# Performance work log

Measured on AMD Instinct MI355X. Metric: run time of the kernel, lower is better.

Reference implementation:

```python
import jax, jax.numpy as jnp
import numpy as np

N = 8192
K = 15


def setup_inputs() -> dict:
    key = jax.random.key(0)
    kx, ky = jax.random.split(key)
    x = jax.random.normal(kx, (N, 2), dtype=jnp.float32)
    y = jax.random.randint(ky, (N,), 0, 2, dtype=jnp.int32)
    return {"x": x, "y": y}


def reference(x, y):
    # Pairwise squared Euclidean distances via ||a||^2 + ||b||^2 - 2 a.b
    n = x.shape[0]
    xx = jnp.sum(x * x, axis=-1)                      # [n]
    d = xx[:, None] + xx[None, :] - 2.0 * (x @ x.T)   # [n, n]
    # exclude self (the original loop skips i == j)
    idx = jnp.arange(n)
    d = d.at[idx, idx].set(jnp.inf)
    # K nearest neighbors per point (smallest distances)
    _, knn_idx = jax.lax.top_k(-d, K)                 # [n, K]
    knn_labels = y[knn_idx].astype(jnp.float32)       # [n, K]
    # majority vote: sum of K binary labels > K/2 -> class 1
    out = (jnp.sum(knn_labels, axis=-1) > (K / 2)).astype(jnp.float32)
    return out
```

## Files before the change

### kernel.cpp

```cpp
#include <hip/hip_runtime.h>

#define NPTS 8192
#define KNN  15
#define QPW  4
#define WPB  8
#define TPB  (WPB * 64)

__device__ __forceinline__ int prefix_below(unsigned long long m) {
  return (int)__builtin_amdgcn_mbcnt_hi((unsigned int)(m >> 32),
            __builtin_amdgcn_mbcnt_lo((unsigned int)m, 0u));
}

__device__ __forceinline__ unsigned int bitonic_sort_u32(unsigned int v, int lane) {
#pragma unroll
  for (int k = 2; k <= 64; k <<= 1) {
#pragma unroll
    for (int j = k >> 1; j > 0; j >>= 1) {
      unsigned int o = __shfl_xor(v, j, 64);
      bool keep_min = ((lane & k) == 0) == ((lane & j) == 0);
      unsigned int lo = (v < o) ? v : o;
      unsigned int hi = (v < o) ? o : v;
      v = keep_min ? lo : hi;
    }
  }
  return v;
}

__device__ __forceinline__ unsigned long long bitonic_sort_u64(unsigned long long v, int lane) {
#pragma unroll
  for (int k = 2; k <= 64; k <<= 1) {
#pragma unroll
    for (int j = k >> 1; j > 0; j >>= 1) {
      unsigned long long o = __shfl_xor(v, j, 64);
      bool keep_min = ((lane & k) == 0) == ((lane & j) == 0);
      unsigned long long lo = (v < o) ? v : o;
      unsigned long long hi = (v < o) ? o : v;
      v = keep_min ? lo : hi;
    }
  }
  return v;
}

__global__ __launch_bounds__(TPB)
void knn_kernel(const float* __restrict__ x, const int* __restrict__ y,
                float* __restrict__ out) {
  __shared__ float4 sx4[NPTS / 2];
  __shared__ unsigned int ybits[NPTS / 32];
  __shared__ unsigned int buf[WPB][QPW][64];

  const int tid = threadIdx.x;

  const float4* gx4 = (const float4*)x;
#pragma unroll
  for (int i = tid; i < NPTS / 2; i += TPB) sx4[i] = gx4[i];
  if (tid < NPTS / 32) {
    const int4* yy = (const int4*)(y + (tid << 5));
    unsigned int b = 0;
#pragma unroll
    for (int k2 = 0; k2 < 8; ++k2) {
      int4 v = yy[k2];
      b |= ((unsigned int)(v.x & 1) << (4 * k2)) |
           ((unsigned int)(v.y & 1) << (4 * k2 + 1)) |
           ((unsigned int)(v.z & 1) << (4 * k2 + 2)) |
           ((unsigned int)(v.w & 1) << (4 * k2 + 3));
    }
    ybits[tid] = b;
  }
  __syncthreads();

  const int w = tid >> 6;
  const int lane = tid & 63;
  const int q0 = ((int)blockIdx.x * WPB + w) * QPW;

  float qx[QPW], qy[QPW];
#pragma unroll
  for (int qi = 0; qi < QPW; ++qi) {
    float2 xq = ((const float2*)sx4)[q0 + qi];
    qx[qi] = xq.x; qy[qi] = xq.y;
  }

  float m0[QPW], m1[QPW];
#pragma unroll
  for (int qi = 0; qi < QPW; ++qi) { m0[qi] = 3.0e38f; m1[qi] = 3.0e38f; }

#pragma unroll 8
  for (int s = 0; s < 64; ++s) {
    float4 p = sx4[(s << 6) + lane];
#pragma unroll
    for (int qi = 0; qi < QPW; ++qi) {
      float dx0 = qx[qi] - p.x, dy0 = qy[qi] - p.y;
      float dx1 = qx[qi] - p.z, dy1 = qy[qi] - p.w;
      float d0 = __builtin_fmaf(dx0, dx0, dy0 * dy0);
      float d1 = __builtin_fmaf(dx1, dx1, dy1 * dy1);
      m0[qi] = fminf(m0[qi], d0);
      m1[qi] = fminf(m1[qi], d1);
    }
  }

  float T[QPW];
#pragma unroll
  for (int qi = 0; qi < QPW; ++qi) {
    unsigned int s = bitonic_sort_u32(__float_as_uint(fminf(m0[qi], m1[qi])), lane);
    T[qi] = __uint_as_float(__shfl(s, KNN, 64)) * (1.0f + 1.0e-5f) + 1.0e-30f;
  }

  int cnt[QPW];
#pragma unroll
  for (int qi = 0; qi < QPW; ++qi) cnt[qi] = 0;

#pragma unroll 4
  for (int s = 0; s < 64; ++s) {
    float4 p = sx4[(s << 6) + lane];
    int j0 = ((s << 6) + lane) << 1;
#pragma unroll
    for (int qi = 0; qi < QPW; ++qi) {
      float dx0 = qx[qi] - p.x, dy0 = qy[qi] - p.y;
      float dx1 = qx[qi] - p.z, dy1 = qy[qi] - p.w;
      float d0 = __builtin_fmaf(dx0, dx0, dy0 * dy0);
      float d1 = __builtin_fmaf(dx1, dx1, dy1 * dy1);
      bool c0 = (d0 <= T[qi]);
      bool c1 = (d1 <= T[qi]);
      unsigned long long k0 = __ballot(c0);
      unsigned long long k1 = __ballot(c1);
      if (k0 | k1) {
        if (c0) {
          int o = cnt[qi] + prefix_below(k0);
          if (o < 64) buf[w][qi][o] = (unsigned)j0;
        }
        if (c1) {
          int o = cnt[qi] + __popcll(k0) + prefix_below(k1);
          if (o < 64) buf[w][qi][o] = (unsigned)(j0 + 1);
        }
        cnt[qi] += __popcll(k0) + __popcll(k1);
      }
    }
  }

#pragma unroll
  for (int qi = 0; qi < QPW; ++qi) {
    const int q = q0 + qi;
    int C = cnt[qi];
    C = (C > 64) ? 64 : C;
    unsigned long long kv = ~0ull;
    if (lane < C) {
      int jj = (int)buf[w][qi][lane];
      float2 pj = ((const float2*)sx4)[jj];
      double dx = (double)qx[qi] - (double)pj.x;
      double dy = (double)qy[qi] - (double)pj.y;
      double dd = dx * dx + dy * dy;
      kv = ((unsigned long long)__double_as_longlong(dd) & ~0x1FFFull) |
           (unsigned long long)jj;
      if (jj == q) kv = ~0ull;
    }
    kv = bitonic_sort_u64(kv, lane);
    int jj = (int)(kv & 0x1FFFull);
    int lbl = (int)((ybits[jj >> 5] >> (jj & 31)) & 1u);
    unsigned long long vm = __ballot((lane < KNN) && lbl);
    if (lane == 0) out[q] = (__popcll(vm) >= 8) ? 1.0f : 0.0f;
  }
}

extern "C" void kernel_launch(void* const* d_in, const int* in_sizes, int n_in,
                              void* d_out, int out_size, void* d_ws, size_t ws_size,
                              hipStream_t stream) {
  const float* x = (const float*)d_in[0];
  const int* y = (const int*)d_in[1];
  float* out = (float*)d_out;
  dim3 grid(NPTS / (WPB * QPW));
  dim3 block(TPB);
  hipLaunchKernelGGL(knn_kernel, grid, block, 0, stream, x, y, out);
}
```

Measured before the change: 38.87 us.

## Split each query group's candidate scan across two waves and merge thresholds in LDS

Each block now holds 4 groups of 4 queries, and each group is served by two waves that each scan half of the points. Per-half sorted minima are combined through shared memory to form a threshold, and candidate lists from both halves are merged before the final sort. The final sorts are spread across both waves (two queries each). The block size stays the same, so the grid doubles and each block reloads all points into LDS, which raises staging cost. It also adds two block barriers and caps each half's candidate list at 48 entries.

```diff
diff --git a/kernel.cpp b/kernel.cpp
--- a/kernel.cpp
+++ b/kernel.cpp
@@ -3,8 +3,9 @@
 #define NPTS 8192
 #define KNN  15
 #define QPW  4
-#define WPB  8
-#define TPB  (WPB * 64)
+#define GPB  4
+#define TPB  512
+#define SEG  48
 
 __device__ __forceinline__ int prefix_below(unsigned long long m) {
   return (int)__builtin_amdgcn_mbcnt_hi((unsigned int)(m >> 32),
@@ -46,7 +47,9 @@
                 float* __restrict__ out) {
   __shared__ float4 sx4[NPTS / 2];
   __shared__ unsigned int ybits[NPTS / 32];
-  __shared__ unsigned int buf[WPB][QPW][64];
+  __shared__ float tmin[GPB][QPW][2][16];
+  __shared__ unsigned int buf[GPB][QPW][2][SEG];
+  __shared__ int cntl[GPB][QPW][2];
 
   const int tid = threadIdx.x;
 
@@ -70,38 +73,55 @@
 
   const int w = tid >> 6;
   const int lane = tid & 63;
-  const int q0 = ((int)blockIdx.x * WPB + w) * QPW;
+  const int g = w & 3;
+  const int h = w >> 2;
+  const int qbase = (int)blockIdx.x * (GPB * QPW) + g * QPW;
 
   float qx[QPW], qy[QPW];
 #pragma unroll
   for (int qi = 0; qi < QPW; ++qi) {
-    float2 xq = ((const float2*)sx4)[q0 + qi];
+    float2 xq = ((const float2*)sx4)[qbase + qi];
     qx[qi] = xq.x; qy[qi] = xq.y;
   }
 
-  float m0[QPW], m1[QPW];
-#pragma unroll
-  for (int qi = 0; qi < QPW; ++qi) { m0[qi] = 3.0e38f; m1[qi] = 3.0e38f; }
+  const float4* base = sx4 + h * (NPTS / 4);
+
+  float m[QPW];
+#pragma unroll
+  for (int qi = 0; qi < QPW; ++qi) m[qi] = 3.0e38f;
 
 #pragma unroll 8
-  for (int s = 0; s < 64; ++s) {
-    float4 p = sx4[(s << 6) + lane];
+  for (int s = 0; s < 32; ++s) {
+    float4 p = base[(s << 6) + lane];
 #pragma unroll
     for (int qi = 0; qi < QPW; ++qi) {
       float dx0 = qx[qi] - p.x, dy0 = qy[qi] - p.y;
       float dx1 = qx[qi] - p.z, dy1 = qy[qi] - p.w;
       float d0 = __builtin_fmaf(dx0, dx0, dy0 * dy0);
       float d1 = __builtin_fmaf(dx1, dx1, dy1 * dy1);
-      m0[qi] = fminf(m0[qi], d0);
-      m1[qi] = fminf(m1[qi], d1);
-    }
-  }
+      m[qi] = fminf(fminf(d0, d1), m[qi]);
+    }
+  }
+
+#pragma unroll
+  for (int qi = 0; qi < QPW; ++qi) {
+    unsigned int srt = bitonic_sort_u32(__float_as_uint(m[qi]), lane);
+    if (lane < 16) tmin[g][qi][h][lane] = __uint_as_float(srt);
+  }
+  __syncthreads();
 
   float T[QPW];
 #pragma unroll
   for (int qi = 0; qi < QPW; ++qi) {
-    unsigned int s = bitonic_sort_u32(__float_as_uint(fminf(m0[qi], m1[qi])), lane);
-    T[qi] = __uint_as_float(__shfl(s, KNN, 64)) * (1.0f + 1.0e-5f) + 1.0e-30f;
+    float cand = 3.0e38f;
+    if (lane <= 16) {
+      float a = (lane == 0) ? 0.0f : tmin[g][qi][0][lane - 1];
+      float b = (lane == 16) ? 0.0f : tmin[g][qi][1][15 - lane];
+      cand = fmaxf(a, b);
+    }
+#pragma unroll
+    for (int j = 32; j >= 1; j >>= 1) cand = fminf(cand, __shfl_xor(cand, j, 64));
+    T[qi] = cand * (1.0f + 1.0e-5f) + 1.0e-30f;
   }
 
   int cnt[QPW];
@@ -109,9 +129,9 @@
   for (int qi = 0; qi < QPW; ++qi) cnt[qi] = 0;
 
 #pragma unroll 4
-  for (int s = 0; s < 64; ++s) {
-    float4 p = sx4[(s << 6) + lane];
-    int j0 = ((s << 6) + lane) << 1;
+  for (int s = 0; s < 32; ++s) {
+    float4 p = base[(s << 6) + lane];
+    int j0 = (h * (NPTS / 4) + (s << 6) + lane) << 1;
 #pragma unroll
     for (int qi = 0; qi < QPW; ++qi) {
       float dx0 = qx[qi] - p.x, dy0 = qy[qi] - p.y;
@@ -125,28 +145,37 @@
       if (k0 | k1) {
         if (c0) {
           int o = cnt[qi] + prefix_below(k0);
-          if (o < 64) buf[w][qi][o] = (unsigned)j0;
+          if (o < SEG) buf[g][qi][h][o] = (unsigned)j0;
         }
         if (c1) {
           int o = cnt[qi] + __popcll(k0) + prefix_below(k1);
-          if (o < 64) buf[w][qi][o] = (unsigned)(j0 + 1);
+          if (o < SEG) buf[g][qi][h][o] = (unsigned)(j0 + 1);
         }
         cnt[qi] += __popcll(k0) + __popcll(k1);
       }
     }
   }
-
-#pragma unroll
-  for (int qi = 0; qi < QPW; ++qi) {
-    const int q = q0 + qi;
-    int C = cnt[qi];
-    C = (C > 64) ? 64 : C;
+  if (lane == 0) {
+    cntl[g][0][h] = cnt[0]; cntl[g][1][h] = cnt[1];
+    cntl[g][2][h] = cnt[2]; cntl[g][3][h] = cnt[3];
+  }
+  __syncthreads();
+
+#pragma unroll
+  for (int t = 0; t < 2; ++t) {
+    const int ql = 2 * h + t;
+    const int q = qbase + ql;
+    const float2 xq = ((const float2*)sx4)[q];
+    int C0 = cntl[g][ql][0]; C0 = (C0 > SEG) ? SEG : C0;
+    int C1 = cntl[g][ql][1]; C1 = (C1 > SEG) ? SEG : C1;
+    int Ct = C0 + C1; Ct = (Ct > 64) ? 64 : Ct;
     unsigned long long kv = ~0ull;
-    if (lane < C) {
-      int jj = (int)buf[w][qi][lane];
+    if (lane < Ct) {
+      int jj = (lane < C0) ? (int)buf[g][ql][0][lane]
+                           : (int)buf[g][ql][1][lane - C0];
       float2 pj = ((const float2*)sx4)[jj];
-      double dx = (double)qx[qi] - (double)pj.x;
-      double dy = (double)qy[qi] - (double)pj.y;
+      double dx = (double)xq.x - (double)pj.x;
+      double dy = (double)xq.y - (double)pj.y;
       double dd = dx * dx + dy * dy;
       kv = ((unsigned long long)__double_as_longlong(dd) & ~0x1FFFull) |
            (unsigned long long)jj;
@@ -166,7 +195,7 @@
   const float* x = (const float*)d_in[0];
   const int* y = (const int*)d_in[1];
   float* out = (float*)d_out;
-  dim3 grid(NPTS / (WPB * QPW));
+  dim3 grid(NPTS / (GPB * QPW));
   dim3 block(TPB);
   hipLaunchKernelGGL(knn_kernel, grid, block, 0, stream, x, y, out);
 }
```

Measured after the change: 33.48 us. 13.9% less time.
